# Kernel optimization log

Hardware: AMD Instinct MI355X
Metric: run time of the kernel (lower is better)

The kernel has to match this reference:

```python
import jax, jax.numpy as jnp
import numpy as np

VOCAB = 100000
EMBED_DIM = 300
TOPK = 10
BATCH = 1024


def setup_inputs() -> dict:
    key = jax.random.key(0)
    k1, k2 = jax.random.split(key)
    wordid = jax.random.randint(k1, (BATCH,), 0, VOCAB, dtype=jnp.int64 if jax.config.jax_enable_x64 else jnp.int32)
    weight = jax.random.normal(k2, (VOCAB, EMBED_DIM), dtype=jnp.float32)
    return {"wordid": wordid, "weight": weight}


def reference(wordid, weight):
    # Embedding lookup: [B, D]
    wordvec = weight[wordid]
    # Dense similarity against full vocab: [B, V]
    sim = jnp.einsum('bd,vd->bv', wordvec, weight)
    # top-(k+1), sorted descending; drop column 0 (the query word itself)
    score, indice = jax.lax.top_k(sim, TOPK + 1)
    return score[:, 1:], indice[:, 1:]
```

## Files before the change

kernel.cpp:

```cpp
#include <hip/hip_runtime.h>
#include <math.h>

#define BATCH 1024
#define VOCAB 100000
#define KDIM  300
#define TOPK  10

#define NKB    10
#define NCB_B  6272
#define NCB_A  64
#define NCC    392
#define NCAND  (NCC*8)
#define NKF    24
#define NDOT   (NKF*4)

typedef __attribute__((ext_vector_type(8))) short bf16x8;
typedef __attribute__((ext_vector_type(4))) float f32x4;
typedef unsigned long long u64;

#define GL2LDS(gsrc, ldst)                                                    \
    __builtin_amdgcn_global_load_lds(                                         \
        (const __attribute__((address_space(1))) void*)(gsrc),                \
        (__attribute__((address_space(3))) void*)(ldst), 16, 0, 0)

__device__ __forceinline__ ushort f2bf(float f) {
    union { float f; unsigned u; } v; v.f = f;
    unsigned r = v.u + 0x7FFFu + ((v.u >> 16) & 1u);
    return (ushort)(r >> 16);
}

__device__ __forceinline__ void ins4(int (&l)[4], int e) {
    if (e <= l[3]) return;
    bool g0 = e > l[0], g1 = e > l[1], g2 = e > l[2];
    l[3] = g2 ? l[2] : e;
    l[2] = g2 ? (g1 ? l[1] : e) : l[2];
    l[1] = g1 ? (g0 ? l[0] : e) : l[1];
    l[0] = g0 ? e : l[0];
}

template<int N>
__device__ __forceinline__ void pins64(u64 (&ks)[N], u64 k) {
    if (k <= ks[N-1]) return;
    #pragma unroll
    for (int p = N-1; p >= 0; --p) {
        bool gt  = k > ks[p];
        bool gtp = (p > 0) ? (k > ks[p-1]) : false;
        ks[p] = gt ? (gtp ? ks[p-1] : k) : ks[p];
    }
}

__global__ __launch_bounds__(256)
void convert_frags(const int* __restrict__ wordid, const float* __restrict__ weight,
                   ushort* __restrict__ ws_b, ushort* __restrict__ ws_a, int nb4)
{
    const int t   = threadIdx.x;
    const int w   = t >> 6, l = t & 63;
    const int bid = blockIdx.x;
    const bool is_a = (bid >= nb4);
    const int cb  = (is_a ? (bid - nb4) : bid) * 4 + w;
    ushort* dst = is_a ? ws_a : ws_b;
    const int kstride = is_a ? 64 : NCB_B;

    const int r16  = l & 15;
    const int ksub = (l >> 4) * 8;

    const int row = is_a ? wordid[cb*16 + r16] : (cb*16 + r16);
    const bool vr = (row < VOCAB);
    const float* src = weight + (size_t)(vr ? row : 0) * KDIM;

    #pragma unroll
    for (int kb = 0; kb < NKB; ++kb) {
        const int k0 = kb*32 + ksub;
        float4 a = make_float4(0.f,0.f,0.f,0.f);
        float4 b = make_float4(0.f,0.f,0.f,0.f);
        if (vr) {
            if (k0 + 8 <= KDIM) {
                a = *reinterpret_cast<const float4*>(src + k0);
                b = *reinterpret_cast<const float4*>(src + k0 + 4);
            } else if (k0 + 4 <= KDIM) {
                a = *reinterpret_cast<const float4*>(src + k0);
            }
        }
        uint4 o;
        o.x = (unsigned)f2bf(a.x) | ((unsigned)f2bf(a.y) << 16);
        o.y = (unsigned)f2bf(a.z) | ((unsigned)f2bf(a.w) << 16);
        o.z = (unsigned)f2bf(b.x) | ((unsigned)f2bf(b.y) << 16);
        o.w = (unsigned)f2bf(b.z) | ((unsigned)f2bf(b.w) << 16);
        *reinterpret_cast<uint4*>(&dst[((size_t)kb*kstride + cb)*512 + (size_t)l*8]) = o;
    }
}

__global__ __launch_bounds__(512, 2)
void sim_gemm(const ushort* __restrict__ ws_a, const ushort* __restrict__ ws_b,
              unsigned* __restrict__ cand)
{
    __shared__ __align__(16) char pool[131072];

    const int id = blockIdx.x;
    const int cc = (id & 7) + ((id >> 5) << 3);
    const int rc = (id >> 3) & 3;

    const int t    = threadIdx.x;
    const int wid  = t >> 6, lane = t & 63;
    const int wm   = wid >> 2, wn = wid & 3;
    const int l16  = lane & 15, lk = lane >> 4;

    auto stage_slot = [&](int kt, int slot, int buf) {
        char* ldst = pool + buf*65536 + slot*1024;
        const ushort* src;
        if (slot < 32) {
            src = ws_a + (((size_t)(kt*2 + (slot>>4))*64) + rc*16 + (slot & 15))*512
                       + (size_t)lane*8;
        } else {
            int s2 = slot - 32;
            src = ws_b + (((size_t)(kt*2 + (s2>>4))*NCB_B) + cc*16 + (s2 & 15))*512
                       + (size_t)lane*8;
        }
        GL2LDS(src, (ushort*)ldst);
    };

    f32x4 acc[8][4] = {};

    #pragma unroll
    for (int j = 0; j < 8; ++j) stage_slot(0, wid*8 + j, 0);
    asm volatile("s_waitcnt vmcnt(0)" ::: "memory");
    __builtin_amdgcn_s_barrier();
    asm volatile("" ::: "memory");

    for (int kt = 0; kt < 5; ++kt) {
        const int buf = kt & 1;
        const ushort* Ab = (const ushort*)(pool + buf*65536);
        const ushort* Bb = (const ushort*)(pool + buf*65536 + 32768);

        if (kt < 4) {
            #pragma unroll
            for (int j = 0; j < 8; ++j)
                stage_slot(kt + 1, wid*8 + j, buf ^ 1);
        }

        bf16x8 bfr[2][4];
        #pragma unroll
        for (int kb = 0; kb < 2; ++kb)
            #pragma unroll
            for (int nf = 0; nf < 4; ++nf)
                bfr[kb][nf] = *reinterpret_cast<const bf16x8*>(
                    Bb + (size_t)(kb*16 + wn*4 + nf)*512 + lane*8);

        #pragma unroll
        for (int p = 0; p < 4; ++p) {
            bf16x8 af[2][2];
            #pragma unroll
            for (int kb = 0; kb < 2; ++kb)
                #pragma unroll
                for (int m2 = 0; m2 < 2; ++m2)
                    af[kb][m2] = *reinterpret_cast<const bf16x8*>(
                        Ab + (size_t)(kb*16 + wm*8 + p*2 + m2)*512 + lane*8);

            __builtin_amdgcn_s_setprio(1);
            #pragma unroll
            for (int m2 = 0; m2 < 2; ++m2)
                #pragma unroll
                for (int nf = 0; nf < 4; ++nf) {
                    acc[p*2+m2][nf] = __builtin_amdgcn_mfma_f32_16x16x32_bf16(
                        bfr[0][nf], af[0][m2], acc[p*2+m2][nf], 0, 0, 0);
                    acc[p*2+m2][nf] = __builtin_amdgcn_mfma_f32_16x16x32_bf16(
                        bfr[1][nf], af[1][m2], acc[p*2+m2][nf], 0, 0, 0);
                }
            __builtin_amdgcn_s_setprio(0);
        }

        if (kt < 4) {
            asm volatile("s_waitcnt vmcnt(0)" ::: "memory");
            __builtin_amdgcn_s_barrier();
            asm volatile("" ::: "memory");
        }
    }

    __syncthreads();
    int* Cls = (int*)pool;
    #pragma unroll
    for (int mf = 0; mf < 8; ++mf) {
        int k0 = 0, k1 = 0;
        #pragma unroll
        for (int nf = 0; nf < 4; ++nf) {
            float qm = fmaxf(fmaxf(acc[mf][nf][0], acc[mf][nf][1]),
                             fmaxf(acc[mf][nf][2], acc[mf][nf][3]));
            int key = (int)((__float_as_uint(qm) & 0xFFFF0000u)
                            | (unsigned)(wn*16 + nf*4 + lk));
            if (key > k0)      { k1 = k0; k0 = key; }
            else if (key > k1) { k1 = key; }
        }
        int row = wm*128 + mf*16 + l16;
        int ent = wn*4 + lk;
        Cls[row*33 + ent*2 + 0] = k0;
        Cls[row*33 + ent*2 + 1] = k1;
    }
    __syncthreads();

    {
        int row  = t >> 1, half = t & 1;
        int ks[4] = {0, 0, 0, 0};
        #pragma unroll
        for (int j = 0; j < 16; ++j)
            ins4(ks, Cls[row*33 + half*16 + j]);
        int grow = rc*256 + row;
        size_t base = (size_t)grow*NCAND + cc*8 + half*4;
        *reinterpret_cast<uint4*>(&cand[base]) =
            make_uint4((unsigned)ks[0], (unsigned)ks[1],
                       (unsigned)ks[2], (unsigned)ks[3]);
    }
}

__global__ __launch_bounds__(256, 8)
void merge_topq(const unsigned* __restrict__ cand, int* __restrict__ quads)
{
    __shared__ u64 Wv[4*NKF];

    const int row  = blockIdx.x;
    const int t    = threadIdx.x;
    const int wid  = t >> 6, lane = t & 63;

    u64 a[13];
    #pragma unroll
    for (int i = 0; i < 13; ++i) a[i] = 0ull;

    const unsigned* rc = cand + (size_t)row*NCAND;
    #pragma unroll
    for (int i = 0; i < 13; ++i) {
        int off = i*64 + lane;
        if (off < 784) {
            int c = wid*784 + off;
            unsigned e = rc[c];
            u64 comb = ((u64)(e ^ 0x80000000u) << 32)
                     | (unsigned)(((c >> 3) << 6) | (e & 63u));
            pins64<13>(a, comb);
        }
    }

    u64 mywin = 0ull;
    for (int k = 0; k < NKF; ++k) {
        u64 h = a[0], r = h;
        #pragma unroll
        for (int m = 1; m < 64; m <<= 1) {
            u64 o = __shfl_xor(r, m);
            r = (o > r) ? o : r;
        }
        bool win = (h == r);
        #pragma unroll
        for (int j = 0; j < 12; ++j) a[j] = win ? a[j+1] : a[j];
        a[12] = win ? 0ull : a[12];
        mywin = (lane == k) ? r : mywin;
    }
    if (lane < NKF) Wv[wid*NKF + lane] = mywin;
    __syncthreads();

    if (wid == 0) {
        u64 b0 = Wv[lane];
        u64 b1 = (lane < 32) ? Wv[lane + 64] : 0ull;
        if (b1 > b0) { u64 tmp = b0; b0 = b1; b1 = tmp; }

        u64 fin = 0ull;
        for (int k = 0; k < NKF; ++k) {
            u64 h = b0, r = h;
            #pragma unroll
            for (int m = 1; m < 64; m <<= 1) {
                u64 o = __shfl_xor(r, m);
                r = (o > r) ? o : r;
            }
            bool win = (h == r);
            b0 = win ? b1 : b0;
            b1 = win ? 0ull : b1;
            fin = (lane == k) ? r : fin;
        }
        if (lane < NKF) quads[row*NKF + lane] = (int)(fin & 0xffffffffull);
    }
}

__global__ __launch_bounds__(256, 8)
void rescore_exact(const int* __restrict__ quads, const int* __restrict__ wordid,
                   const float* __restrict__ weight, double* __restrict__ scores)
{
    const int g = (blockIdx.x * 256 + threadIdx.x) >> 4;
    const int l = threadIdx.x & 15;
    const int row = g / NDOT;
    const int ci  = g - row * NDOT;

    const int q   = quads[row*NKF + (ci >> 2)];
    const int col = q*4 + (ci & 3);
    const bool valid = (col < VOCAB);
    const int col_eff = valid ? col : 0;

    const float* qr = weight + (size_t)wordid[row]*KDIM;
    const float* wr = weight + (size_t)col_eff*KDIM;

    double a0 = 0.0, a1 = 0.0;
    #pragma unroll
    for (int k = 0; k < 4; ++k) {
        int sl = (l + 16*k) * 4;
        float4 qa = *reinterpret_cast<const float4*>(qr + sl);
        float4 wb = *reinterpret_cast<const float4*>(wr + sl);
        a0 += (double)qa.x * wb.x + (double)qa.z * wb.z;
        a1 += (double)qa.y * wb.y + (double)qa.w * wb.w;
    }
    if (l < 11) {
        int sl = (l + 64) * 4;
        float4 qa = *reinterpret_cast<const float4*>(qr + sl);
        float4 wb = *reinterpret_cast<const float4*>(wr + sl);
        a0 += (double)qa.x * wb.x + (double)qa.z * wb.z;
        a1 += (double)qa.y * wb.y + (double)qa.w * wb.w;
    }
    double a = a0 + a1;
    #pragma unroll
    for (int m = 1; m < 16; m <<= 1) a += __shfl_xor(a, m);

    if (l == 0) scores[g] = valid ? a : -1e300;
}

__global__ __launch_bounds__(64, 8)
void final_select(const double* __restrict__ scores, const int* __restrict__ quads,
                  float* __restrict__ out)
{
    const int row  = blockIdx.x;
    const int lane = threadIdx.x;

    double v0 = -INFINITY, v1 = -INFINITY;
    int    c0 = 0x7fffffff, c1 = 0x7fffffff;
    if (lane < NDOT/2) {
        int i0 = lane*2, i1 = lane*2 + 1;
        v0 = scores[(size_t)row*NDOT + i0];
        v1 = scores[(size_t)row*NDOT + i1];
        c0 = quads[row*NKF + (i0 >> 2)]*4 + (i0 & 3);
        c1 = quads[row*NKF + (i1 >> 2)]*4 + (i1 & 3);
    }

    for (int kk = 0; kk < TOPK + 1; ++kk) {
        bool sel = (v0 > v1) || (v0 == v1 && c0 < c1);
        double bv = sel ? v0 : v1;
        int    bc = sel ? c0 : c1;
        #pragma unroll
        for (int m = 1; m < 64; m <<= 1) {
            double ov = __shfl_xor(bv, m);
            int    oc = __shfl_xor(bc, m);
            if (ov > bv || (ov == bv && oc < bc)) { bv = ov; bc = oc; }
        }
        if (kk >= 1 && lane == 0) {
            out[(size_t)row*TOPK + (kk-1)] = (float)bv;
            out[(size_t)BATCH*TOPK + (size_t)row*TOPK + (kk-1)] = (float)bc;
        }
        if (c0 == bc) v0 = -INFINITY;
        if (c1 == bc) v1 = -INFINITY;
    }
}

extern "C" void kernel_launch(void* const* d_in, const int* in_sizes, int n_in,
                              void* d_out, int out_size, void* d_ws, size_t ws_size,
                              hipStream_t stream) {
    const int*   wordid = (const int*)d_in[0];
    const float* weight = (const float*)d_in[1];
    float* out = (float*)d_out;

    const size_t SZ_B = (size_t)NCB_B * NKB * 64 * 16;
    const size_t SZ_A = (size_t)NCB_A * NKB * 64 * 16;

    char* p = (char*)d_ws;
    ushort*   ws_b = (ushort*)p;  p += SZ_B;
    ushort*   ws_a = (ushort*)p;  p += SZ_A;
    unsigned* cand = (unsigned*)p;

    int*    quads  = (int*)ws_a;
    double* scores = (double*)cand;

    convert_frags<<<NCB_B/4 + NCB_A/4, 256, 0, stream>>>(wordid, weight, ws_b, ws_a, NCB_B/4);
    sim_gemm<<<NCC*4, 512, 0, stream>>>(ws_a, ws_b, cand);
    merge_topq<<<BATCH, 256, 0, stream>>>(cand, quads);
    rescore_exact<<<(BATCH*NDOT)/16, 256, 0, stream>>>(quads, wordid, weight, scores);
    final_select<<<BATCH, 64, 0, stream>>>(scores, quads, out);
}
```

Measured before the change: 182.7 us.

## Load B fragments directly from global into registers, halve LDS footprint

The B operand tiles no longer go through LDS. Each wave loads its B fragments from global memory straight into registers and double-buffers them across k-steps, while A is still staged in LDS. This halves LDS use per block and drops the LDS round trip for B, which could raise occupancy. In exchange, register pressure rises from two B fragment sets, and the full unroll of the k-loop makes the code larger.

```diff
diff --git a/kernel.cpp b/kernel.cpp
--- a/kernel.cpp
+++ b/kernel.cpp
@@ -94,7 +94,7 @@
 void sim_gemm(const ushort* __restrict__ ws_a, const ushort* __restrict__ ws_b,
               unsigned* __restrict__ cand)
 {
-    __shared__ __align__(16) char pool[131072];
+    __shared__ __align__(16) char pool[65536];
 
     const int id = blockIdx.x;
     const int cc = (id & 7) + ((id >> 5) << 3);
@@ -105,46 +105,48 @@
     const int wm   = wid >> 2, wn = wid & 3;
     const int l16  = lane & 15, lk = lane >> 4;
 
-    auto stage_slot = [&](int kt, int slot, int buf) {
-        char* ldst = pool + buf*65536 + slot*1024;
-        const ushort* src;
-        if (slot < 32) {
-            src = ws_a + (((size_t)(kt*2 + (slot>>4))*64) + rc*16 + (slot & 15))*512
-                       + (size_t)lane*8;
-        } else {
-            int s2 = slot - 32;
-            src = ws_b + (((size_t)(kt*2 + (s2>>4))*NCB_B) + cc*16 + (s2 & 15))*512
-                       + (size_t)lane*8;
-        }
-        GL2LDS(src, (ushort*)ldst);
+    auto stageA = [&](int kt, int buf) {
+        #pragma unroll
+        for (int j = 0; j < 4; ++j) {
+            const int slot = wid*4 + j;
+            char* ldst = pool + buf*32768 + slot*1024;
+            const ushort* src = ws_a
+                + ((size_t)(kt*2 + (slot>>4))*64 + rc*16 + (slot & 15))*512
+                + (size_t)lane*8;
+            GL2LDS(src, (ushort*)ldst);
+        }
     };
 
+    auto loadB = [&](int kt, bf16x8 (&b)[2][4]) {
+        #pragma unroll
+        for (int kb = 0; kb < 2; ++kb)
+            #pragma unroll
+            for (int nf = 0; nf < 4; ++nf)
+                b[kb][nf] = *reinterpret_cast<const bf16x8*>(
+                    ws_b + ((size_t)(kt*2 + kb)*NCB_B + cc*16 + wn*4 + nf)*512
+                         + (size_t)lane*8);
+    };
+
     f32x4 acc[8][4] = {};
-
-    #pragma unroll
-    for (int j = 0; j < 8; ++j) stage_slot(0, wid*8 + j, 0);
+    bf16x8 bA[2][4], bB[2][4];
+
+    stageA(0, 0);
+    loadB(0, bA);
     asm volatile("s_waitcnt vmcnt(0)" ::: "memory");
     __builtin_amdgcn_s_barrier();
     asm volatile("" ::: "memory");
 
+    #pragma unroll
     for (int kt = 0; kt < 5; ++kt) {
         const int buf = kt & 1;
-        const ushort* Ab = (const ushort*)(pool + buf*65536);
-        const ushort* Bb = (const ushort*)(pool + buf*65536 + 32768);
+        const ushort* Ab = (const ushort*)(pool + buf*32768);
+        bf16x8 (&bcur)[2][4] = (kt & 1) ? bB : bA;
+        bf16x8 (&bnxt)[2][4] = (kt & 1) ? bA : bB;
 
         if (kt < 4) {
-            #pragma unroll
-            for (int j = 0; j < 8; ++j)
-                stage_slot(kt + 1, wid*8 + j, buf ^ 1);
-        }
-
-        bf16x8 bfr[2][4];
-        #pragma unroll
-        for (int kb = 0; kb < 2; ++kb)
-            #pragma unroll
-            for (int nf = 0; nf < 4; ++nf)
-                bfr[kb][nf] = *reinterpret_cast<const bf16x8*>(
-                    Bb + (size_t)(kb*16 + wn*4 + nf)*512 + lane*8);
+            stageA(kt + 1, buf ^ 1);
+            loadB(kt + 1, bnxt);
+        }
 
         #pragma unroll
         for (int p = 0; p < 4; ++p) {
@@ -162,9 +164,9 @@
                 #pragma unroll
                 for (int nf = 0; nf < 4; ++nf) {
                     acc[p*2+m2][nf] = __builtin_amdgcn_mfma_f32_16x16x32_bf16(
-                        bfr[0][nf], af[0][m2], acc[p*2+m2][nf], 0, 0, 0);
+                        bcur[0][nf], af[0][m2], acc[p*2+m2][nf], 0, 0, 0);
                     acc[p*2+m2][nf] = __builtin_amdgcn_mfma_f32_16x16x32_bf16(
-                        bfr[1][nf], af[1][m2], acc[p*2+m2][nf], 0, 0, 0);
+                        bcur[1][nf], af[1][m2], acc[p*2+m2][nf], 0, 0, 0);
                 }
             __builtin_amdgcn_s_setprio(0);
         }
```

Result: slower. 187.8 us (+2.8%).
